# Kernel tuning notes

Hardware: AMD Instinct MI355X
Metric: run time of the kernel (lower is better)

The kernel has to match this reference:

```python
import jax, jax.numpy as jnp
import numpy as np

N_NODES = 100000
N_EDGES = 1600000
D_IN = 128
D_OUT = 64
NUM_LAYERS = 3
BN_EPS = 1e-5


def setup_inputs() -> dict:
    key = jax.random.key(0)
    k_x, k_e, k_w = jax.random.split(key, 3)
    x = jax.random.normal(k_x, (N_NODES, D_IN), dtype=jnp.float32)
    edge_index = jax.random.randint(k_e, (2, N_EDGES), 0, N_NODES, dtype=jnp.int64)
    bn_gamma = jnp.ones((NUM_LAYERS, D_IN), dtype=jnp.float32)
    bn_beta = jnp.zeros((NUM_LAYERS, D_IN), dtype=jnp.float32)
    W = jax.random.normal(k_w, (D_IN, D_OUT), dtype=jnp.float32) * (1.0 / np.sqrt(D_IN))
    b = jnp.zeros((D_OUT,), dtype=jnp.float32)
    return {"x": x, "edge_index": edge_index, "bn_gamma": bn_gamma, "bn_beta": bn_beta, "W": W, "b": b}


def reference(x, edge_index, bn_gamma, bn_beta, W, b):
    # GNN forward, task='node', aggregate='sum', combine='sum', readout='sum',
    # recursive_weighting=False, training mode (no sigmoid, BN uses batch stats).
    n = x.shape[0]
    dst = edge_index[0]  # spmm(Adj, h): pooled[i] = sum over edges (i <- j) of h[j]
    src = edge_index[1]
    h = x
    for layer in range(NUM_LAYERS):
        # neighbor aggregate: sparse spmm == gather + segment-sum scatter
        agg = jax.ops.segment_sum(h[src], dst, num_segments=n)  # [N, D]
        # graph readout (single batched graph): sum over nodes, broadcast to every node
        readout = jnp.sum(h, axis=0, keepdims=True)  # [1, D]
        # functional 'sum' combine of (self, aggregated, readout)
        h = h + agg + readout
        # BatchNorm1d over the node dimension (training statistics, biased var)
        mean = jnp.mean(h, axis=0)
        var = jnp.var(h, axis=0)
        h = (h - mean) * jax.lax.rsqrt(var + BN_EPS) * bn_gamma[layer] + bn_beta[layer]
        h = jax.nn.relu(h)
    # node-task head (training branch: raw logits)
    return h @ W + b
```

## Files before the change

### kernel.cpp

```cpp
#include <hip/hip_runtime.h>

#define D 128
#define DOUT 64
#define BN_EPS 1e-5f
#define BCAP 96

#define NBK_SHIFT 8
#define NBK_MAX   512
#define SLOT_CAP  704
#define PA_E      4000

typedef unsigned int   u32;
typedef unsigned short u16;
typedef short  short8 __attribute__((ext_vector_type(8)));
typedef float  f32x4  __attribute__((ext_vector_type(4)));

__device__ __forceinline__ u16 f2bf(float f) {
    u32 x = __float_as_uint(f);
    x += 0x7fffu + ((x >> 16) & 1u);
    return (u16)(x >> 16);
}
__device__ __forceinline__ float bflo(u32 u) { return __uint_as_float(u << 16); }
__device__ __forceinline__ float bfhi(u32 u) { return __uint_as_float(u & 0xffff0000u); }

__global__ void init_kernel(const float* __restrict__ x, u16* __restrict__ xb,
                            int* __restrict__ bcnt,
                            float* __restrict__ stats,
                            const float* __restrict__ W, u16* __restrict__ wt,
                            int n_nodes, int n_ctr) {
    int total = n_nodes * (D / 4);
    for (int t = blockIdx.x * blockDim.x + threadIdx.x; t < total;
         t += gridDim.x * blockDim.x) {
        float4 v = ((const float4*)x)[t];
        ((ushort4*)xb)[t] = make_ushort4(f2bf(v.x), f2bf(v.y), f2bf(v.z), f2bf(v.w));
        if (t < n_ctr) bcnt[t] = 0;
        if (t < 2048) stats[t] = (t >= 256 && t < 384) ? 1.f : 0.f;
        if (t < D * DOUT) {
            int c = t >> 7, k = t & (D - 1);
            wt[t] = f2bf(W[k * DOUT + c]);
        }
    }
}

__global__ __launch_bounds__(256) void partA_kernel(const int* __restrict__ ei,
                             int* __restrict__ bcnt,
                             u32* __restrict__ pairs, int n_edges, int n_bkt) {
    __shared__ u32 ord[PA_E];
    __shared__ u16 obkt[PA_E];
    __shared__ int hist[NBK_MAX];
    __shared__ int scanA[NBK_MAX], scanB[NBK_MAX];
    __shared__ int st[NBK_MAX], cur[NBK_MAX], gbase[NBK_MAX];

    const int tid  = threadIdx.x;
    const int slot = blockIdx.x & 7;
    const int e0   = blockIdx.x * PA_E;
    const int e1   = min(e0 + PA_E, n_edges);

    for (int i = tid; i < NBK_MAX; i += 256) hist[i] = 0;
    __syncthreads();
    for (int e = e0 + tid; e < e1; e += 256)
        atomicAdd(&hist[ei[e] >> NBK_SHIFT], 1);
    __syncthreads();
    for (int i = tid; i < NBK_MAX; i += 256) scanA[i] = hist[i];
    __syncthreads();
    int* a = scanA; int* b = scanB;
    for (int s = 1; s < NBK_MAX; s <<= 1) {
        for (int i = tid; i < NBK_MAX; i += 256)
            b[i] = a[i] + (i >= s ? a[i - s] : 0);
        __syncthreads();
        int* t_ = a; a = b; b = t_;
    }
    for (int x = tid; x < n_bkt; x += 256) {
        int c   = hist[x];
        int stx = a[x] - c;
        st[x] = stx; cur[x] = stx;
        gbase[x] = c ? atomicAdd(&bcnt[((x << 3) + slot) << 4], c) : 0;
    }
    __syncthreads();
    for (int e = e0 + tid; e < e1; e += 256) {
        int d = ei[e];
        int s = ei[n_edges + e];
        int x = d >> NBK_SHIFT;
        int pos = atomicAdd(&cur[x], 1);
        ord[pos]  = ((u32)(d & 255) << 17) | (u32)s;
        obkt[pos] = (u16)x;
    }
    __syncthreads();
    const int cntE = e1 - e0;
    for (int i = tid; i < cntE; i += 256) {
        int x   = obkt[i];
        int pos = gbase[x] + (i - st[x]);
        if (pos < SLOT_CAP)
            pairs[(size_t)((x << 3) + slot) * SLOT_CAP + pos] = ord[i];
    }
}

__global__ __launch_bounds__(256) void partB_kernel(const u32* __restrict__ pairs,
                             const int* __restrict__ bcnt,
                             int* __restrict__ deg, int* __restrict__ srcs,
                             int n_nodes) {
    __shared__ u32 lp[8 * SLOT_CAP];
    __shared__ int lsrc[8 * SLOT_CAP];
    __shared__ int cnt[256], st[256], cur[256];
    __shared__ int scanA[256], scanB[256];
    __shared__ int sofs[9];
    const int tid = threadIdx.x;
    int b = blockIdx.x;
    int node0 = b << NBK_SHIFT;
    if (tid == 0) {
        int acc = 0;
        for (int x = 0; x < 8; ++x) {
            sofs[x] = acc;
            acc += min(bcnt[((b << 3) + x) << 4], SLOT_CAP);
        }
        sofs[8] = acc;
    }
    cnt[tid] = 0;
    __syncthreads();
    for (int x = 0; x < 8; ++x) {
        int c0 = sofs[x], c1 = sofs[x + 1];
        const u32* src = pairs + (size_t)((b << 3) + x) * SLOT_CAP;
        for (int t = tid; t < c1 - c0; t += blockDim.x) {
            u32 pr = src[t];
            lp[c0 + t] = pr;
            atomicAdd(&cnt[pr >> 17], 1);
        }
    }
    __syncthreads();
    scanA[tid] = cnt[tid];
    __syncthreads();
    int* a = scanA; int* bb = scanB;
    for (int s = 1; s < 256; s <<= 1) {
        bb[tid] = a[tid] + (tid >= s ? a[tid - s] : 0);
        __syncthreads();
        int* t_ = a; a = bb; bb = t_;
    }
    st[tid] = a[tid] - cnt[tid];
    cur[tid] = st[tid];
    __syncthreads();
    int cntE = sofs[8];
    for (int t = tid; t < cntE; t += blockDim.x) {
        u32 pr = lp[t];
        int pos = atomicAdd(&cur[pr >> 17], 1);
        lsrc[pos] = (int)(pr & 0x1FFFFu);
    }
    __syncthreads();
    int grp = tid >> 4, lane = tid & 15;
    for (int li = grp; li < 256; li += 16) {
        int node = node0 + li;
        if (node < n_nodes) {
            int dg = cnt[li], s0 = st[li];
            for (int t = lane; t < dg; t += 16) {
                int key = lsrc[s0 + t];
                int rank = 0;
                for (int u = 0; u < dg; ++u) {
                    int o = lsrc[s0 + u];
                    rank += (o < key) || (o == key && u < t);
                }
                if (rank < BCAP) srcs[(size_t)node * BCAP + rank] = key;
            }
            if (lane == 0) deg[node] = dg;
        }
    }
}

template <bool APPLY>
__global__ void agg_kernel(const u16* __restrict__ h,
                           const int* __restrict__ srcs,
                           const int* __restrict__ deg,
                           const float* __restrict__ stats_prev,
                           u16* __restrict__ vout,
                           int n_nodes) {
    const int lane = threadIdx.x & 15;
    const int grp  = threadIdx.x >> 4;
    const int c    = lane << 3;
    float sc[8], sh[8];
    #pragma unroll
    for (int k = 0; k < 8; ++k) {
        sc[k] = stats_prev[256 + c + k];
        sh[k] = stats_prev[384 + c + k];
    }
    const int stride = gridDim.x * 16;
    float a[8];

#define ACC(u_) do { \
    float f0 = bflo((u_).x), f1 = bfhi((u_).x); \
    float f2 = bflo((u_).y), f3 = bfhi((u_).y); \
    float f4 = bflo((u_).z), f5 = bfhi((u_).z); \
    float f6 = bflo((u_).w), f7 = bfhi((u_).w); \
    if (APPLY) { \
        a[0] += fmaxf(fmaf(f0, sc[0], sh[0]), 0.f); \
        a[1] += fmaxf(fmaf(f1, sc[1], sh[1]), 0.f); \
        a[2] += fmaxf(fmaf(f2, sc[2], sh[2]), 0.f); \
        a[3] += fmaxf(fmaf(f3, sc[3], sh[3]), 0.f); \
        a[4] += fmaxf(fmaf(f4, sc[4], sh[4]), 0.f); \
        a[5] += fmaxf(fmaf(f5, sc[5], sh[5]), 0.f); \
        a[6] += fmaxf(fmaf(f6, sc[6], sh[6]), 0.f); \
        a[7] += fmaxf(fmaf(f7, sc[7], sh[7]), 0.f); \
    } else { \
        a[0] += f0; a[1] += f1; a[2] += f2; a[3] += f3; \
        a[4] += f4; a[5] += f5; a[6] += f6; a[7] += f7; \
    } } while (0)

    for (int i = blockIdx.x * 16 + grp; i < n_nodes; i += stride) {
        int off = i * BCAP;
        int dg  = min(deg[i], BCAP);
        {
            uint4 u = *(const uint4*)(h + ((size_t)i << 7) + c);
            float f0 = bflo(u.x), f1 = bfhi(u.x), f2 = bflo(u.y), f3 = bfhi(u.y);
            float f4 = bflo(u.z), f5 = bfhi(u.z), f6 = bflo(u.w), f7 = bfhi(u.w);
            float ff[8] = {f0, f1, f2, f3, f4, f5, f6, f7};
            #pragma unroll
            for (int k = 0; k < 8; ++k)
                a[k] = APPLY ? fmaxf(fmaf(ff[k], sc[k], sh[k]), 0.f) : ff[k];
        }
        for (int base = 0; base < dg; base += 16) {
            int cnt = min(dg - base, 16);
            int sv = (lane < cnt) ? srcs[off + base + lane] : 0;
            int k = 0;
            for (; k + 4 <= cnt; k += 4) {
                int j0 = __shfl(sv, k + 0, 16), j1 = __shfl(sv, k + 1, 16);
                int j2 = __shfl(sv, k + 2, 16), j3 = __shfl(sv, k + 3, 16);
                uint4 b0 = *(const uint4*)(h + ((size_t)j0 << 7) + c);
                uint4 b1 = *(const uint4*)(h + ((size_t)j1 << 7) + c);
                uint4 b2 = *(const uint4*)(h + ((size_t)j2 << 7) + c);
                uint4 b3 = *(const uint4*)(h + ((size_t)j3 << 7) + c);
                ACC(b0); ACC(b1); ACC(b2); ACC(b3);
            }
            for (; k < cnt; ++k) {
                int j0 = __shfl(sv, k, 16);
                uint4 b0 = *(const uint4*)(h + ((size_t)j0 << 7) + c);
                ACC(b0);
            }
        }
        uint4 w;
        w.x = (u32)f2bf(a[0]) | ((u32)f2bf(a[1]) << 16);
        w.y = (u32)f2bf(a[2]) | ((u32)f2bf(a[3]) << 16);
        w.z = (u32)f2bf(a[4]) | ((u32)f2bf(a[5]) << 16);
        w.w = (u32)f2bf(a[6]) | ((u32)f2bf(a[7]) << 16);
        *(uint4*)(vout + ((size_t)i << 7) + c) = w;
    }
#undef ACC
}

__global__ void stats_kernel(const u16* __restrict__ v,
                             float* __restrict__ stats_cur, int n_nodes) {
    int col = threadIdx.x & 63;
    int sub = threadIdx.x >> 6;
    float s1a = 0.f, s1b = 0.f, s2a = 0.f, s2b = 0.f;
    const u32* vp = (const u32*)v;
    for (int r = blockIdx.x * 4 + sub; r < n_nodes; r += gridDim.x * 4) {
        u32 w = vp[(size_t)r * 64 + col];
        float fa = bflo(w), fb = bfhi(w);
        s1a += fa; s1b += fb; s2a += fa * fa; s2b += fb * fb;
    }
    __shared__ float red[4][64][4];
    red[sub][col][0] = s1a; red[sub][col][1] = s1b;
    red[sub][col][2] = s2a; red[sub][col][3] = s2b;
    __syncthreads();
    if (sub == 0) {
        #pragma unroll
        for (int m = 1; m < 4; ++m) {
            red[0][col][0] += red[m][col][0];
            red[0][col][1] += red[m][col][1];
            red[0][col][2] += red[m][col][2];
            red[0][col][3] += red[m][col][3];
        }
        unsafeAtomicAdd(&stats_cur[2 * col + 0], red[0][col][0]);
        unsafeAtomicAdd(&stats_cur[2 * col + 1], red[0][col][1]);
        unsafeAtomicAdd(&stats_cur[128 + 2 * col + 0], red[0][col][2]);
        unsafeAtomicAdd(&stats_cur[128 + 2 * col + 1], red[0][col][3]);
    }
}

__global__ void finalize_stats_kernel(float* __restrict__ stats_cur,
                                      const float* __restrict__ gamma,
                                      const float* __restrict__ beta,
                                      int layer, float inv_n) {
    int f = threadIdx.x;
    float mean = stats_cur[f] * inv_n;
    float var  = stats_cur[128 + f] * inv_n - mean * mean;
    var = fmaxf(var, 0.f);
    float s = gamma[layer * D + f] * rsqrtf(var + BN_EPS);
    stats_cur[256 + f] = s;
    stats_cur[384 + f] = beta[layer * D + f] - mean * s;
}

__global__ __launch_bounds__(256) void head_mfma_kernel(
        const u16* __restrict__ v2, const float* __restrict__ stats3,
        const u16* __restrict__ wt, const float* __restrict__ b,
        float* __restrict__ out, int n_nodes) {
    const int wave = threadIdx.x >> 6;
    const int lane = threadIdx.x & 63;
    const int lo   = lane & 15;
    const int hi   = lane >> 4;

    short8 Bf[4][4];
    #pragma unroll
    for (int ct = 0; ct < 4; ++ct)
        #pragma unroll
        for (int ks = 0; ks < 4; ++ks)
            Bf[ct][ks] = *(const short8*)(wt + (ct * 16 + lo) * D + ks * 32 + hi * 8);

    float sc[4][8], sh[4][8];
    #pragma unroll
    for (int ks = 0; ks < 4; ++ks)
        #pragma unroll
        for (int j = 0; j < 8; ++j) {
            int f = ks * 32 + hi * 8 + j;
            sc[ks][j] = stats3[256 + f];
            sh[ks][j] = stats3[384 + f];
        }
    float bias[4];
    #pragma unroll
    for (int ct = 0; ct < 4; ++ct) bias[ct] = b[ct * 16 + lo];

    const int nrt = (n_nodes + 15) >> 4;
    for (int rt = blockIdx.x * 4 + wave; rt < nrt; rt += gridDim.x * 4) {
        const int r0 = rt << 4;
        const int ar = min(r0 + lo, n_nodes - 1);
        const u16* hrow = v2 + ((size_t)ar << 7);
        f32x4 acc[4];
        #pragma unroll
        for (int ct = 0; ct < 4; ++ct) acc[ct] = (f32x4){0.f, 0.f, 0.f, 0.f};
        #pragma unroll
        for (int ks = 0; ks < 4; ++ks) {
            uint4 u = *(const uint4*)(hrow + ks * 32 + hi * 8);
            float f0 = bflo(u.x), f1 = bfhi(u.x), f2 = bflo(u.y), f3 = bfhi(u.y);
            float f4 = bflo(u.z), f5 = bfhi(u.z), f6 = bflo(u.w), f7 = bfhi(u.w);
            float w0 = fmaxf(fmaf(f0, sc[ks][0], sh[ks][0]), 0.f);
            float w1 = fmaxf(fmaf(f1, sc[ks][1], sh[ks][1]), 0.f);
            float w2 = fmaxf(fmaf(f2, sc[ks][2], sh[ks][2]), 0.f);
            float w3 = fmaxf(fmaf(f3, sc[ks][3], sh[ks][3]), 0.f);
            float w4 = fmaxf(fmaf(f4, sc[ks][4], sh[ks][4]), 0.f);
            float w5 = fmaxf(fmaf(f5, sc[ks][5], sh[ks][5]), 0.f);
            float w6 = fmaxf(fmaf(f6, sc[ks][6], sh[ks][6]), 0.f);
            float w7 = fmaxf(fmaf(f7, sc[ks][7], sh[ks][7]), 0.f);
            union { uint4 u4; short8 s8; } af;
            af.u4.x = (u32)f2bf(w0) | ((u32)f2bf(w1) << 16);
            af.u4.y = (u32)f2bf(w2) | ((u32)f2bf(w3) << 16);
            af.u4.z = (u32)f2bf(w4) | ((u32)f2bf(w5) << 16);
            af.u4.w = (u32)f2bf(w6) | ((u32)f2bf(w7) << 16);
            #pragma unroll
            for (int ct = 0; ct < 4; ++ct)
                acc[ct] = __builtin_amdgcn_mfma_f32_16x16x32_bf16(
                    af.s8, Bf[ct][ks], acc[ct], 0, 0, 0);
        }
        #pragma unroll
        for (int ct = 0; ct < 4; ++ct)
            #pragma unroll
            for (int rg = 0; rg < 4; ++rg) {
                int r = r0 + hi * 4 + rg;
                if (r < n_nodes)
                    out[(size_t)r * DOUT + ct * 16 + lo] = acc[ct][rg] + bias[ct];
            }
    }
}

extern "C" void kernel_launch(void* const* d_in, const int* in_sizes, int n_in,
                              void* d_out, int out_size, void* d_ws, size_t ws_size,
                              hipStream_t stream) {
    const float* x     = (const float*)d_in[0];
    const int*   ei    = (const int*)d_in[1];
    const float* gamma = (const float*)d_in[2];
    const float* beta  = (const float*)d_in[3];
    const float* W     = (const float*)d_in[4];
    const float* bvec  = (const float*)d_in[5];
    float* out = (float*)d_out;

    const int n_nodes = in_sizes[0] / D;
    const int n_edges = in_sizes[1] / 2;
    const int n_bkt   = (n_nodes + 255) >> 8;
    const int n_ctr   = n_bkt * 8 * 16;

    const size_t row_bytes = (size_t)n_nodes * D * sizeof(u16);
    char* p = (char*)d_ws;
    u16*   xb     = (u16*)p;   p += row_bytes;
    u16*   vA     = (u16*)p;   p += row_bytes;
    u16*   vB     = (u16*)p;   p += row_bytes;
    int*   srcs   = (int*)p;   p += (size_t)n_nodes * BCAP * sizeof(int);
    int*   deg    = (int*)p;   p += (size_t)n_nodes * sizeof(int);
    int*   bcnt   = (int*)p;   p += (size_t)n_ctr * sizeof(int);
    float* stats  = (float*)p;
    u16*   Wt     = (u16*)(p + 2048 * sizeof(float));
    u32* pairs  = (u32*)vB;

    const float inv_n = 1.0f / (float)n_nodes;

    init_kernel<<<2048, 256, 0, stream>>>(x, xb, bcnt, stats, W, Wt, n_nodes, n_ctr);
    int pa_grid = ((n_edges + PA_E - 1) / PA_E + 7) & ~7;
    partA_kernel<<<pa_grid, 256, 0, stream>>>(ei, bcnt, pairs, n_edges, n_bkt);
    partB_kernel<<<n_bkt, 256, 0, stream>>>(pairs, bcnt, deg, srcs, n_nodes);

    const u16* h = xb;
    u16* vout = vA;
    for (int L = 0; L < 3; ++L) {
        float* scur = stats + (size_t)(L + 1) * 512;
        const float* sprev = stats + (size_t)L * 512;
        if (L == 0)
            agg_kernel<false><<<4096, 256, 0, stream>>>(h, srcs, deg,
                sprev, vout, n_nodes);
        else
            agg_kernel<true><<<4096, 256, 0, stream>>>(h, srcs, deg,
                sprev, vout, n_nodes);
        stats_kernel<<<512, 256, 0, stream>>>(vout, scur, n_nodes);
        finalize_stats_kernel<<<1, D, 0, stream>>>(scur, gamma, beta, L, inv_n);
        h = vout;
        vout = (vout == vA) ? vB : vA;
    }

    head_mfma_kernel<<<782, 256, 0, stream>>>(h, stats + 3 * 512, Wt, bvec,
                                              out, n_nodes);
}
```

Before: 501.4 us.

## Fuse BatchNorm statistics into aggregation kernel and drop separate stats passes

The aggregation kernel now accumulates per-feature sum and sum-of-squares from its fp32 outputs and reduces them through shared memory. Each block then adds its totals with atomics into one of 8 partial buffers to spread contention. The consumer kernels (next aggregation layer and head) fold those partials into BN scale and shift themselves, so the separate stats and finalize kernels are removed. The gather loop also gains an 8-wide unrolled path and a prefetch of the next neighbor-index chunk. Risks: 4096x256-entry atomics per layer, redundant scale/shift computation in every thread, and stats now taken from fp32 values rather than the rounded bf16 outputs.

```diff
diff --git a/kernel.cpp b/kernel.cpp
--- a/kernel.cpp
+++ b/kernel.cpp
@@ -25,7 +25,7 @@
 
 __global__ void init_kernel(const float* __restrict__ x, u16* __restrict__ xb,
                             int* __restrict__ bcnt,
-                            float* __restrict__ stats,
+                            float* __restrict__ sums,
                             const float* __restrict__ W, u16* __restrict__ wt,
                             int n_nodes, int n_ctr) {
     int total = n_nodes * (D / 4);
@@ -34,7 +34,7 @@
         float4 v = ((const float4*)x)[t];
         ((ushort4*)xb)[t] = make_ushort4(f2bf(v.x), f2bf(v.y), f2bf(v.z), f2bf(v.w));
         if (t < n_ctr) bcnt[t] = 0;
-        if (t < 2048) stats[t] = (t >= 256 && t < 384) ? 1.f : 0.f;
+        if (t < 3 * 8 * 256) sums[t] = 0.f;
         if (t < D * DOUT) {
             int c = t >> 7, k = t & (D - 1);
             wt[t] = f2bf(W[k * DOUT + c]);
@@ -168,20 +168,36 @@
 __global__ void agg_kernel(const u16* __restrict__ h,
                            const int* __restrict__ srcs,
                            const int* __restrict__ deg,
-                           const float* __restrict__ stats_prev,
+                           const float* __restrict__ sums_prev,
+                           const float* __restrict__ gam,
+                           const float* __restrict__ bet,
+                           float* __restrict__ sums_out,
                            u16* __restrict__ vout,
-                           int n_nodes) {
+                           int n_nodes, float inv_n) {
     const int lane = threadIdx.x & 15;
     const int grp  = threadIdx.x >> 4;
     const int c    = lane << 3;
     float sc[8], sh[8];
-    #pragma unroll
-    for (int k = 0; k < 8; ++k) {
-        sc[k] = stats_prev[256 + c + k];
-        sh[k] = stats_prev[384 + c + k];
+    if (APPLY) {
+        #pragma unroll
+        for (int k = 0; k < 8; ++k) {
+            int f = c + k;
+            float S = 0.f, Q = 0.f;
+            #pragma unroll
+            for (int cp = 0; cp < 8; ++cp) {
+                S += sums_prev[cp * 256 + f];
+                Q += sums_prev[cp * 256 + 128 + f];
+            }
+            float mean = S * inv_n;
+            float var  = fmaxf(Q * inv_n - mean * mean, 0.f);
+            sc[k] = gam[f] * rsqrtf(var + BN_EPS);
+            sh[k] = bet[f] - mean * sc[k];
+        }
     }
     const int stride = gridDim.x * 16;
     float a[8];
+    float s1[8] = {0,0,0,0,0,0,0,0};
+    float s2[8] = {0,0,0,0,0,0,0,0};
 
 #define ACC(u_) do { \
     float f0 = bflo((u_).x), f1 = bfhi((u_).x); \
@@ -217,7 +233,26 @@
         for (int base = 0; base < dg; base += 16) {
             int cnt = min(dg - base, 16);
             int sv = (lane < cnt) ? srcs[off + base + lane] : 0;
+            int svn = 0;
+            int nb = base + 16;
+            if (nb < dg && lane < min(dg - nb, 16)) svn = srcs[off + nb + lane];
             int k = 0;
+            for (; k + 8 <= cnt; k += 8) {
+                int j0 = __shfl(sv, k + 0, 16), j1 = __shfl(sv, k + 1, 16);
+                int j2 = __shfl(sv, k + 2, 16), j3 = __shfl(sv, k + 3, 16);
+                int j4 = __shfl(sv, k + 4, 16), j5 = __shfl(sv, k + 5, 16);
+                int j6 = __shfl(sv, k + 6, 16), j7 = __shfl(sv, k + 7, 16);
+                uint4 b0 = *(const uint4*)(h + ((size_t)j0 << 7) + c);
+                uint4 b1 = *(const uint4*)(h + ((size_t)j1 << 7) + c);
+                uint4 b2 = *(const uint4*)(h + ((size_t)j2 << 7) + c);
+                uint4 b3 = *(const uint4*)(h + ((size_t)j3 << 7) + c);
+                uint4 b4 = *(const uint4*)(h + ((size_t)j4 << 7) + c);
+                uint4 b5 = *(const uint4*)(h + ((size_t)j5 << 7) + c);
+                uint4 b6 = *(const uint4*)(h + ((size_t)j6 << 7) + c);
+                uint4 b7 = *(const uint4*)(h + ((size_t)j7 << 7) + c);
+                ACC(b0); ACC(b1); ACC(b2); ACC(b3);
+                ACC(b4); ACC(b5); ACC(b6); ACC(b7);
+            }
             for (; k + 4 <= cnt; k += 4) {
                 int j0 = __shfl(sv, k + 0, 16), j1 = __shfl(sv, k + 1, 16);
                 int j2 = __shfl(sv, k + 2, 16), j3 = __shfl(sv, k + 3, 16);
@@ -232,6 +267,7 @@
                 uint4 b0 = *(const uint4*)(h + ((size_t)j0 << 7) + c);
                 ACC(b0);
             }
+            sv = svn;
         }
         uint4 w;
         w.x = (u32)f2bf(a[0]) | ((u32)f2bf(a[1]) << 16);
@@ -239,57 +275,38 @@
         w.z = (u32)f2bf(a[4]) | ((u32)f2bf(a[5]) << 16);
         w.w = (u32)f2bf(a[6]) | ((u32)f2bf(a[7]) << 16);
         *(uint4*)(vout + ((size_t)i << 7) + c) = w;
+        #pragma unroll
+        for (int k = 0; k < 8; ++k) {
+            s1[k] += a[k];
+            s2[k] = fmaf(a[k], a[k], s2[k]);
+        }
     }
 #undef ACC
-}
-
-__global__ void stats_kernel(const u16* __restrict__ v,
-                             float* __restrict__ stats_cur, int n_nodes) {
-    int col = threadIdx.x & 63;
-    int sub = threadIdx.x >> 6;
-    float s1a = 0.f, s1b = 0.f, s2a = 0.f, s2b = 0.f;
-    const u32* vp = (const u32*)v;
-    for (int r = blockIdx.x * 4 + sub; r < n_nodes; r += gridDim.x * 4) {
-        u32 w = vp[(size_t)r * 64 + col];
-        float fa = bflo(w), fb = bfhi(w);
-        s1a += fa; s1b += fb; s2a += fa * fa; s2b += fb * fb;
-    }
-    __shared__ float red[4][64][4];
-    red[sub][col][0] = s1a; red[sub][col][1] = s1b;
-    red[sub][col][2] = s2a; red[sub][col][3] = s2b;
-    __syncthreads();
-    if (sub == 0) {
-        #pragma unroll
-        for (int m = 1; m < 4; ++m) {
-            red[0][col][0] += red[m][col][0];
-            red[0][col][1] += red[m][col][1];
-            red[0][col][2] += red[m][col][2];
-            red[0][col][3] += red[m][col][3];
-        }
-        unsafeAtomicAdd(&stats_cur[2 * col + 0], red[0][col][0]);
-        unsafeAtomicAdd(&stats_cur[2 * col + 1], red[0][col][1]);
-        unsafeAtomicAdd(&stats_cur[128 + 2 * col + 0], red[0][col][2]);
-        unsafeAtomicAdd(&stats_cur[128 + 2 * col + 1], red[0][col][3]);
-    }
-}
-
-__global__ void finalize_stats_kernel(float* __restrict__ stats_cur,
-                                      const float* __restrict__ gamma,
-                                      const float* __restrict__ beta,
-                                      int layer, float inv_n) {
-    int f = threadIdx.x;
-    float mean = stats_cur[f] * inv_n;
-    float var  = stats_cur[128 + f] * inv_n - mean * mean;
-    var = fmaxf(var, 0.f);
-    float s = gamma[layer * D + f] * rsqrtf(var + BN_EPS);
-    stats_cur[256 + f] = s;
-    stats_cur[384 + f] = beta[layer * D + f] - mean * s;
+
+    __shared__ float redS[16][128];
+    __shared__ float redQ[16][128];
+    #pragma unroll
+    for (int k = 0; k < 8; ++k) {
+        redS[grp][c + k] = s1[k];
+        redQ[grp][c + k] = s2[k];
+    }
+    __syncthreads();
+    int tid = threadIdx.x;
+    if (tid < 128) {
+        float S = 0.f, Q = 0.f;
+        #pragma unroll
+        for (int g = 0; g < 16; ++g) { S += redS[g][tid]; Q += redQ[g][tid]; }
+        int cp = blockIdx.x & 7;
+        unsafeAtomicAdd(&sums_out[cp * 256 + tid], S);
+        unsafeAtomicAdd(&sums_out[cp * 256 + 128 + tid], Q);
+    }
 }
 
 __global__ __launch_bounds__(256) void head_mfma_kernel(
-        const u16* __restrict__ v2, const float* __restrict__ stats3,
+        const u16* __restrict__ v2, const float* __restrict__ sums2,
+        const float* __restrict__ gam, const float* __restrict__ bet,
         const u16* __restrict__ wt, const float* __restrict__ b,
-        float* __restrict__ out, int n_nodes) {
+        float* __restrict__ out, int n_nodes, float inv_n) {
     const int wave = threadIdx.x >> 6;
     const int lane = threadIdx.x & 63;
     const int lo   = lane & 15;
@@ -308,8 +325,16 @@
         #pragma unroll
         for (int j = 0; j < 8; ++j) {
             int f = ks * 32 + hi * 8 + j;
-            sc[ks][j] = stats3[256 + f];
-            sh[ks][j] = stats3[384 + f];
+            float S = 0.f, Q = 0.f;
+            #pragma unroll
+            for (int cp = 0; cp < 8; ++cp) {
+                S += sums2[cp * 256 + f];
+                Q += sums2[cp * 256 + 128 + f];
+            }
+            float mean = S * inv_n;
+            float var  = fmaxf(Q * inv_n - mean * mean, 0.f);
+            sc[ks][j] = gam[f] * rsqrtf(var + BN_EPS);
+            sh[ks][j] = bet[f] - mean * sc[ks][j];
         }
     float bias[4];
     #pragma unroll
@@ -381,13 +406,13 @@
     int*   srcs   = (int*)p;   p += (size_t)n_nodes * BCAP * sizeof(int);
     int*   deg    = (int*)p;   p += (size_t)n_nodes * sizeof(int);
     int*   bcnt   = (int*)p;   p += (size_t)n_ctr * sizeof(int);
-    float* stats  = (float*)p;
-    u16*   Wt     = (u16*)(p + 2048 * sizeof(float));
+    float* sums   = (float*)p;
+    u16*   Wt     = (u16*)(p + 3 * 8 * 256 * sizeof(float));
     u32* pairs  = (u32*)vB;
 
     const float inv_n = 1.0f / (float)n_nodes;
 
-    init_kernel<<<2048, 256, 0, stream>>>(x, xb, bcnt, stats, W, Wt, n_nodes, n_ctr);
+    init_kernel<<<2048, 256, 0, stream>>>(x, xb, bcnt, sums, W, Wt, n_nodes, n_ctr);
     int pa_grid = ((n_edges + PA_E - 1) / PA_E + 7) & ~7;
     partA_kernel<<<pa_grid, 256, 0, stream>>>(ei, bcnt, pairs, n_edges, n_bkt);
     partB_kernel<<<n_bkt, 256, 0, stream>>>(pairs, bcnt, deg, srcs, n_nodes);
@@ -395,20 +420,20 @@
     const u16* h = xb;
     u16* vout = vA;
     for (int L = 0; L < 3; ++L) {
-        float* scur = stats + (size_t)(L + 1) * 512;
-        const float* sprev = stats + (size_t)L * 512;
+        float* sout = sums + (size_t)L * 2048;
+        const float* sprev = (L > 0) ? sums + (size_t)(L - 1) * 2048 : nullptr;
         if (L == 0)
             agg_kernel<false><<<4096, 256, 0, stream>>>(h, srcs, deg,
-                sprev, vout, n_nodes);
+                nullptr, nullptr, nullptr, sout, vout, n_nodes, inv_n);
         else
             agg_kernel<true><<<4096, 256, 0, stream>>>(h, srcs, deg,
-                sprev, vout, n_nodes);
-        stats_kernel<<<512, 256, 0, stream>>>(vout, scur, n_nodes);
-        finalize_stats_kernel<<<1, D, 0, stream>>>(scur, gamma, beta, L, inv_n);
+                sprev, gamma + (size_t)(L - 1) * D, beta + (size_t)(L - 1) * D,
+                sout, vout, n_nodes, inv_n);
         h = vout;
         vout = (vout == vA) ? vB : vA;
     }
 
-    head_mfma_kernel<<<782, 256, 0, stream>>>(h, stats + 3 * 512, Wt, bvec,
-                                              out, n_nodes);
-}
+    head_mfma_kernel<<<782, 256, 0, stream>>>(h, sums + 2 * 2048,
+                                              gamma + 2 * D, beta + 2 * D,
+                                              Wt, bvec, out, n_nodes, inv_n);
+}
```

New measurement: 515.5 us. +2.8%, slower.
